# Kernel tuning notes

Hardware: AMD Instinct MI355X
Metric: run time of the kernel (lower is better)

## Reference

```python
import jax, jax.numpy as jnp
import numpy as np

# ---- dims (see shape_source) ----
B_IMG, R, E = 64, 36, 1024          # images: (n_image, n_regions, embed_size)
C_CAP, L, N_DEP = 64, 32, 30        # captions: (n_caption, n_word, embed_size)
NUM_BLOCK = 32                      # opt.num_block -> tnode feature dim (= feat_dim)
BLK = E // NUM_BLOCK                # n_block = embed_size // num_block
HID = 512                           # hid_dim (divisible by n_kernels=8)
LAM = 9.0                           # opt.lambda_softmax
EPS = 1e-8


def l2norm(x, axis):
    return x / (jnp.sqrt(jnp.sum(x * x, axis=axis, keepdims=True)) + EPS)


def setup_inputs() -> dict:
    key = jax.random.key(0)
    k = jax.random.split(key, 9)
    return {
        "images": jax.random.normal(k[0], (B_IMG, R, E), jnp.float32),
        "captions": jax.random.normal(k[1], (C_CAP, L, E), jnp.float32),
        "depends": jax.random.randint(k[2], (C_CAP, N_DEP, 2), 0, L, dtype=jnp.int32),
        # TextQueryGraphConvolution: n_kernels blocks of (HID//n_kernels, feat) concat == one (HID, feat) matrix, bias=False
        "W_gc": jax.random.normal(k[3], (HID, NUM_BLOCK), jnp.float32) / np.float32(np.sqrt(NUM_BLOCK)),
        "W_mu": jax.random.normal(k[4], (HID, HID), jnp.float32) / np.float32(np.sqrt(HID)),
        "b_mu": jnp.zeros((HID,), jnp.float32),
        "W_lv": jax.random.normal(k[5], (HID, HID), jnp.float32) * np.float32(0.02),
        "b_lv": jnp.zeros((HID,), jnp.float32),
        "W1": jax.random.normal(k[6], (HID, HID), jnp.float32) / np.float32(np.sqrt(HID)),
        "b1": jnp.zeros((HID,), jnp.float32),
        "W2": jax.random.normal(k[7], (1, HID), jnp.float32) / np.float32(np.sqrt(HID)),
        "b2": jnp.zeros((1,), jnp.float32),
    }


def _forward(images, captions, depends, W_gc, W_mu, b_mu, W_lv, b_lv, W1, b1, W2, b2):
    dep_mask = (jnp.arange(N_DEP) > 0).astype(jnp.float32)  # build_sparse_graph skips pair i==0
    eye = jnp.eye(L, dtype=jnp.float32)

    def per_caption(cap, dep):            # cap: (L,E), dep: (N_DEP,2) int
        # intra_relations: softmax over keys of lam * (Q K^T)
        words_sim = jax.nn.softmax(LAM * (cap @ cap.T), axis=-1)            # (L,L)
        # inter_relations(images, cap): leakyrelu -> l2norm over words -> softmax over regions
        attn = jnp.einsum('bre,le->brl', images, cap)                       # (B,R,L)
        attn = jnp.where(attn >= 0, attn, 0.1 * attn)                       # LeakyReLU(0.1)
        attn = l2norm(attn, axis=2)
        attn = jax.nn.softmax(LAM * jnp.swapaxes(attn, 1, 2), axis=-1)      # (B,L,R)
        wctx = jnp.einsum('blr,bre->ble', attn, images)                     # weighted context (B,L,E)
        # node-level matching: blockwise cosine similarity
        q = jnp.broadcast_to(cap, (B_IMG, L, E)).reshape(B_IMG, L, NUM_BLOCK, BLK)
        c = wctx.reshape(B_IMG, L, NUM_BLOCK, BLK)
        num = jnp.sum(q * c, axis=-1)
        den = jnp.maximum(jnp.linalg.norm(q, axis=-1) * jnp.linalg.norm(c, axis=-1), EPS)
        tnode = num / den                                                   # (B,L,NUM_BLOCK)
        # build_sparse_graph: symmetric 0/1 scatter (skip pair 0) + I
        adj = jnp.zeros((L, L), jnp.float32)
        adj = adj.at[dep[:, 0], dep[:, 1]].max(dep_mask)
        adj = adj.at[dep[:, 1], dep[:, 0]].max(dep_mask)
        adj = adj + eye
        # neighbor weights: l2norm over neighbor axis of adj-masked intra relations
        nw = l2norm(adj * words_sim, axis=1)                                # (L,L)
        # graph conv: neighbor_nodes[b,j,n,f] = adj[j,n]*tnode[b,j,f] (broadcast of unsqueeze(2));
        # agg[b,j,f] = sum_n nw[j,n]*adj[j,n]*tnode[b,j,f]; then block-concat linear = (HID,F) matmul
        s = jnp.sum(nw * adj, axis=1)                                       # (L,)
        hidden = (tnode * s[None, :, None]) @ W_gc.T                        # (B,L,HID)
        # Gaussian-process head; RBF kernel diagonal of K(x,x) is exp(0)=1, so sigma unchanged
        mu = hidden @ W_mu.T + b_mu
        sigma = jnp.exp(0.5 * (hidden @ W_lv.T + b_lv)) * 1.0
        h2 = jnp.tanh(hidden @ W1.T + b1)
        sim = (h2 @ W2.T + b2).reshape(B_IMG, L).mean(axis=1)               # (B,)
        return sim, mu, sigma

    sims, t_m, t_s = jax.vmap(per_caption)(captions, depends)               # (C,B), (C,B,L,H)
    similarities = sims.T                                                   # (B,C)
    t_m = jnp.swapaxes(t_m, 0, 1)                                           # (B,C,L,H)
    t_s = jnp.swapaxes(t_s, 0, 1)
    w = jax.nn.softmax(similarities, axis=1)[:, :, None, None]
    mu_word = jnp.sum(w * t_m, axis=1)
    var_word = jnp.sum(w * (t_s ** 2 + t_m ** 2), axis=1) - mu_word ** 2
    sigma_word = jnp.sqrt(jnp.maximum(var_word, 1e-8))
    return similarities, mu_word, sigma_word


def reference(images, captions, depends, W_gc, W_mu, b_mu, W_lv, b_lv, W1, b1, W2, b2):
    return _forward(images, captions, depends, W_gc, W_mu, b_mu, W_lv, b_lv, W1, b1, W2, b2)
```

## Files before the change

kernel.cpp:

```cpp
#include <hip/hip_runtime.h>
#include <math.h>

#define LAM 9.0f
#define EPSF 1e-8f

typedef unsigned int uint;
typedef unsigned short ushort_t;
typedef __attribute__((ext_vector_type(8))) short short8;
typedef __attribute__((ext_vector_type(4))) float float4v;
typedef __attribute__((ext_vector_type(16))) float f32x16;

#define OFF_MMU 0
#define OFF_MLV (512*32)
#define OFF_M1  (2*512*32)
#define OFF_S   (3*512*32)
#define OFF_W   (OFF_S + 64*32)
#define OFF_QN  (OFF_W + 64*64)
#define OFF_TS  (OFF_QN + 64*32*32)
#define OFF_ATTN (OFF_TS + 64*64*32*32)
#define OFF_CVT  (OFF_ATTN + 2304*2048)

#define N_IMG_EL 2359296
#define N_CAP_EL 2097152
#define IMGT2_EL 3145728

__device__ __forceinline__ ushort_t bf16_rne(float x) {
    uint u = __float_as_uint(x);
    uint r = (u + 0x7fffu + ((u >> 16) & 1u)) >> 16;
    return (ushort_t)r;
}
__device__ __forceinline__ float bf16_f(ushort_t h) {
    return __uint_as_float(((uint)h) << 16);
}
__device__ __forceinline__ uint pack2(ushort_t a, ushort_t b) {
    return (uint)a | ((uint)b << 16);
}

__global__ __launch_bounds__(256) void kcvt(const float* __restrict__ img,
                                            const float* __restrict__ cap,
                                            ushort_t* __restrict__ dst) {
    size_t i = (size_t)blockIdx.x * 256 + threadIdx.x;
    const float* src;
    ushort_t *H, *L;
    size_t base;
    if (i < (N_IMG_EL / 4)) {
        src = img; H = dst; L = dst + N_IMG_EL; base = i * 4;
    } else {
        src = cap; H = dst + 2 * (size_t)N_IMG_EL; L = H + N_CAP_EL; base = (i - N_IMG_EL / 4) * 4;
    }
    float4 v = *(const float4*)(src + base);
    float x[4] = {v.x, v.y, v.z, v.w};
    ushort_t hh[4], ll[4];
    #pragma unroll
    for (int j = 0; j < 4; j++) {
        hh[j] = bf16_rne(x[j]);
        ll[j] = bf16_rne(x[j] - bf16_f(hh[j]));
    }
    *(uint2*)(H + base) = make_uint2(pack2(hh[0], hh[1]), pack2(hh[2], hh[3]));
    *(uint2*)(L + base) = make_uint2(pack2(ll[0], ll[1]), pack2(ll[2], ll[3]));
}

__global__ __launch_bounds__(256) void kcvt2(const float* __restrict__ img,
                                             ushort_t* __restrict__ dstH) {
    int b = blockIdx.x >> 3, ecg = blockIdx.x & 7;
    __shared__ float S[36][132];
    int t = threadIdx.x;
    for (int i = t; i < 1152; i += 256) {
        int r = i >> 5, q = i & 31;
        *(float4*)&S[r][q * 4] = *(const float4*)(img + ((size_t)b * 36 + r) * 1024 + ecg * 128 + q * 4);
    }
    __syncthreads();
    int lane = t & 63, grp = t >> 6;
    int m = lane & 31, hi = lane >> 5;
    #pragma unroll
    for (int w2 = 0; w2 < 3; w2++) {
        int item = grp + w2 * 4;
        int estepL = item / 3;
        int ks3 = item - estepL * 3;
        ushort_t hh[8], ll[8];
        #pragma unroll
        for (int j = 0; j < 8; j++) {
            int r = ks3 * 16 + hi * 8 + j;
            float v = (r < 36) ? S[r][estepL * 32 + m] : 0.f;
            hh[j] = bf16_rne(v);
            ll[j] = bf16_rne(v - bf16_f(hh[j]));
        }
        int estep = ecg * 4 + estepL;
        size_t off = ((((size_t)b * 32 + estep) * 3 + ks3) * 64 + lane) * 8;
        uint4 uh, ul;
        uh.x = pack2(hh[0], hh[1]); uh.y = pack2(hh[2], hh[3]);
        uh.z = pack2(hh[4], hh[5]); uh.w = pack2(hh[6], hh[7]);
        ul.x = pack2(ll[0], ll[1]); ul.y = pack2(ll[2], ll[3]);
        ul.z = pack2(ll[4], ll[5]); ul.w = pack2(ll[6], ll[7]);
        *(uint4*)(dstH + off) = uh;
        *(uint4*)(dstH + IMGT2_EL + off) = ul;
    }
}

__global__ __launch_bounds__(256) void k2a_mfma(const ushort_t* __restrict__ cvt,
                                                float* __restrict__ C) {
    const ushort_t* imgH = cvt;
    const ushort_t* imgL = cvt + N_IMG_EL;
    const ushort_t* capH = cvt + 2 * (size_t)N_IMG_EL;
    const ushort_t* capL = capH + N_CAP_EL;
    __shared__ ushort_t Ah[128][32], Al[128][32], Bh[64][32], Bl[64][32];
    int t = threadIdx.x, w = t >> 6, lane = t & 63;
    int quad = lane >> 4, mn = lane & 15;
    int m0 = blockIdx.x * 128, n0 = blockIdx.y * 64;
    float4v acc[2][4];
    #pragma unroll
    for (int i = 0; i < 2; i++)
        #pragma unroll
        for (int j = 0; j < 4; j++) acc[i][j] = (float4v){0.f, 0.f, 0.f, 0.f};

    for (int kc = 0; kc < 32; kc++) {
        #pragma unroll
        for (int j = 0; j < 6; j++) {
            int ch = t + j * 256;
            const ushort_t* src;
            ushort_t* dst;
            if (ch < 512) {
                int row = ch >> 2, seg = ch & 3;
                src = imgH + (size_t)(m0 + row) * 1024 + kc * 32 + seg * 8;
                dst = &Ah[0][0] + ch * 8;
            } else if (ch < 1024) {
                int r2 = ch - 512, row = r2 >> 2, seg = r2 & 3;
                src = imgL + (size_t)(m0 + row) * 1024 + kc * 32 + seg * 8;
                dst = &Al[0][0] + r2 * 8;
            } else if (ch < 1280) {
                int r2 = ch - 1024, row = r2 >> 2, seg = r2 & 3;
                src = capH + (size_t)(n0 + row) * 1024 + kc * 32 + seg * 8;
                dst = &Bh[0][0] + r2 * 8;
            } else {
                int r2 = ch - 1280, row = r2 >> 2, seg = r2 & 3;
                src = capL + (size_t)(n0 + row) * 1024 + kc * 32 + seg * 8;
                dst = &Bl[0][0] + r2 * 8;
            }
            __builtin_amdgcn_global_load_lds(
                (const __attribute__((address_space(1))) uint*)src,
                (__attribute__((address_space(3))) uint*)dst, 16, 0, 0);
        }
        __syncthreads();
        short8 ah[2], al[2];
        #pragma unroll
        for (int tm = 0; tm < 2; tm++) {
            ah[tm] = *(short8*)&Ah[w * 32 + tm * 16 + mn][quad * 8];
            al[tm] = *(short8*)&Al[w * 32 + tm * 16 + mn][quad * 8];
        }
        #pragma unroll
        for (int nt = 0; nt < 4; nt++) {
            short8 bh = *(short8*)&Bh[nt * 16 + mn][quad * 8];
            short8 bl = *(short8*)&Bl[nt * 16 + mn][quad * 8];
            #pragma unroll
            for (int tm = 0; tm < 2; tm++) {
                acc[tm][nt] = __builtin_amdgcn_mfma_f32_16x16x32_bf16(ah[tm], bh, acc[tm][nt], 0, 0, 0);
                acc[tm][nt] = __builtin_amdgcn_mfma_f32_16x16x32_bf16(ah[tm], bl, acc[tm][nt], 0, 0, 0);
                acc[tm][nt] = __builtin_amdgcn_mfma_f32_16x16x32_bf16(al[tm], bh, acc[tm][nt], 0, 0, 0);
            }
        }
        __syncthreads();
    }
    #pragma unroll
    for (int tm = 0; tm < 2; tm++)
        #pragma unroll
        for (int nt = 0; nt < 4; nt++)
            #pragma unroll
            for (int r = 0; r < 4; r++) {
                int mrow = m0 + w * 32 + tm * 16 + quad * 4 + r;
                int ncol = n0 + nt * 16 + mn;
                C[(size_t)mrow * 2048 + ncol] = acc[tm][nt][r];
            }
}

__global__ __launch_bounds__(256) void kpre(const float* __restrict__ Wmu,
                                            const float* __restrict__ Wlv,
                                            const float* __restrict__ W1,
                                            const float* __restrict__ Wgc,
                                            float* __restrict__ ws) {
    int m = blockIdx.x >> 6;
    int hg = blockIdx.x & 63;
    int h0 = hg * 8;
    const float* W = (m == 0) ? Wmu : (m == 1) ? Wlv : W1;
    __shared__ float Gs[64][32];
    __shared__ float Ws[8][68];
    int t = threadIdx.x;
    int h = t >> 5, f = t & 31;
    float acc = 0.f;
    for (int kc = 0; kc < 8; kc++) {
        for (int i = t; i < 512; i += 256) {
            int row = i >> 3, c4 = i & 7;
            *(float4*)&Gs[row][c4 * 4] = *(const float4*)(Wgc + (kc * 64 + row) * 32 + c4 * 4);
        }
        if (t < 128) {
            int hh = t >> 4, c4 = t & 15;
            *(float4*)&Ws[hh][c4 * 4] = *(const float4*)(W + (size_t)(h0 + hh) * 512 + kc * 64 + c4 * 4);
        }
        __syncthreads();
        #pragma unroll 4
        for (int k = 0; k < 64; k++) acc += Ws[h][k] * Gs[k][f];
        __syncthreads();
    }
    ushort_t* Mb = (ushort_t*)ws + m * 32768;
    ushort_t hi = bf16_rne(acc);
    ushort_t lo = bf16_rne(acc - bf16_f(hi));
    Mb[(h0 + h) * 32 + f] = hi;
    Mb[16384 + (h0 + h) * 32 + f] = lo;
}

__global__ __launch_bounds__(256) void k1(const float* __restrict__ captions,
                                          const int* __restrict__ depends,
                                          float* __restrict__ ws) {
    int c = blockIdx.x;
    __shared__ float caps[32][65];
    __shared__ float G[32][33];
    __shared__ float adj[32][33];
    int t = threadIdx.x;
    int l2 = t & 31, l1_0 = t >> 5;
    float acc[4] = {0.f, 0.f, 0.f, 0.f};
    const float* cap = captions + (size_t)c * 32 * 1024;

    for (int kc = 0; kc < 16; kc++) {
        for (int i = t; i < 512; i += 256) {
            int ll = i >> 4, q = i & 15;
            float4 v = *(const float4*)(cap + ll * 1024 + kc * 64 + q * 4);
            caps[ll][q * 4 + 0] = v.x; caps[ll][q * 4 + 1] = v.y;
            caps[ll][q * 4 + 2] = v.z; caps[ll][q * 4 + 3] = v.w;
        }
        __syncthreads();
        #pragma unroll 4
        for (int k = 0; k < 64; k++) {
            float cv = caps[l2][k];
            #pragma unroll
            for (int i = 0; i < 4; i++) acc[i] += caps[l1_0 + 8 * i][k] * cv;
        }
        __syncthreads();
    }
    #pragma unroll
    for (int i = 0; i < 4; i++) G[l1_0 + 8 * i][l2] = acc[i];
    for (int i = t; i < 32 * 33; i += 256) ((float*)adj)[i] = 0.f;
    __syncthreads();

    if (t < 32) {
        float mx = -1e30f;
        for (int n = 0; n < 32; n++) mx = fmaxf(mx, LAM * G[t][n]);
        float sum = 0.f;
        for (int n = 0; n < 32; n++) { float p = __expf(LAM * G[t][n] - mx); G[t][n] = p; sum += p; }
        float inv = 1.f / sum;
        for (int n = 0; n < 32; n++) G[t][n] *= inv;
    }
    __syncthreads();
    if (t >= 1 && t < 30) {
        int d0 = depends[c * 60 + t * 2 + 0];
        int d1 = depends[c * 60 + t * 2 + 1];
        adj[d0][d1] = 1.f;
        adj[d1][d0] = 1.f;
    }
    __syncthreads();
    if (t < 32) adj[t][t] += 1.f;
    __syncthreads();
    if (t < 32) {
        float ss = 0.f, sw = 0.f;
        for (int n = 0; n < 32; n++) { float mm = adj[t][n] * G[t][n]; ss += mm * mm; }
        float inv = 1.f / (sqrtf(ss) + EPSF);
        for (int n = 0; n < 32; n++) sw += adj[t][n] * G[t][n] * adj[t][n];
        ws[OFF_S + c * 32 + t] = sw * inv;
    }
    for (int p = t; p < 1024; p += 256) {
        int l = p >> 5, f = p & 31;
        const float* cp = cap + (size_t)l * 1024 + f * 32;
        float q2 = 0.f;
        #pragma unroll
        for (int q = 0; q < 8; q++) {
            float4 v = *(const float4*)(cp + q * 4);
            q2 += v.x * v.x + v.y * v.y + v.z * v.z + v.w * v.w;
        }
        ws[OFF_QN + c * 1024 + p] = sqrtf(q2);
    }
}

__global__ __launch_bounds__(256) void k2a(const float* __restrict__ A,
                                           const float* __restrict__ Bm,
                                           float* __restrict__ C,
                                           int n0, int NW) {
    __shared__ float As[16][132];
    __shared__ float Bs[16][68];
    int m0 = blockIdx.x * 128;
    int nb0 = n0 + blockIdx.y * 64;
    int t = threadIdx.x;
    int tm = t >> 4, tn = t & 15;
    float acc[8][4] = {};
    for (int kc = 0; kc < 64; kc++) {
        #pragma unroll
        for (int j = 0; j < 2; j++) {
            int idx = t + j * 256;
            int row = idx >> 2, kq = idx & 3;
            float4 v = *(const float4*)(A + (size_t)(m0 + row) * 1024 + kc * 16 + kq * 4);
            As[kq * 4 + 0][row] = v.x; As[kq * 4 + 1][row] = v.y;
            As[kq * 4 + 2][row] = v.z; As[kq * 4 + 3][row] = v.w;
        }
        {
            int row = t >> 2, kq = t & 3;
            float4 v = *(const float4*)(Bm + (size_t)(nb0 + row) * 1024 + kc * 16 + kq * 4);
            Bs[kq * 4 + 0][row] = v.x; Bs[kq * 4 + 1][row] = v.y;
            Bs[kq * 4 + 2][row] = v.z; Bs[kq * 4 + 3][row] = v.w;
        }
        __syncthreads();
        #pragma unroll
        for (int kk = 0; kk < 16; kk++) {
            float a0[4], a1[4], bb[4];
            *(float4*)a0 = *(float4*)&As[kk][tm * 8];
            *(float4*)a1 = *(float4*)&As[kk][tm * 8 + 4];
            *(float4*)bb = *(float4*)&Bs[kk][tn * 4];
            #pragma unroll
            for (int i = 0; i < 4; i++)
                #pragma unroll
                for (int j2 = 0; j2 < 4; j2++) {
                    acc[i][j2]     += a0[i] * bb[j2];
                    acc[i + 4][j2] += a1[i] * bb[j2];
                }
        }
        __syncthreads();
    }
    int cw0 = nb0 - n0 + tn * 4;
    #pragma unroll
    for (int i = 0; i < 8; i++) {
        float4 v = make_float4(acc[i][0], acc[i][1], acc[i][2], acc[i][3]);
        *(float4*)(C + (size_t)(m0 + tm * 8 + i) * NW + cw0) = v;
    }
}

__global__ __launch_bounds__(64) void k2bm(const ushort_t* __restrict__ imgT,
                                           const float* __restrict__ captions,
                                           const float* __restrict__ attn,
                                           const float* __restrict__ ws,
                                           float* __restrict__ ts_out) {
    int orig = blockIdx.x;
    int fh = orig >> 10;
    int rest = orig & 1023;
    int cpair = rest >> 5;
    int bp = rest & 31;
    int b0 = bp * 2;
    int c0 = cpair * 2;
    __shared__ union {
        float A[2][2][36][33];
        float T[2][2][16][33];
    } u;
    int t = threadIdx.x;
    int l = t & 31, hi = t >> 5;

    for (int i = t; i < 1152; i += 64) {
        int bi = i >= 576;
        int i2 = i - bi * 576;
        int ci = i2 >= 288;
        int i3 = i2 - ci * 288;
        int r = i3 >> 3, q = i3 & 7;
        *(float4*)&u.A[bi][ci][r][q * 4] =
            *(const float4*)(attn + (size_t)((b0 + bi) * 36 + r) * 2048 + (c0 + ci) * 32 + q * 4);
    }
    __syncthreads();
    for (int i = t; i < 144; i += 64) {
        int bi = i >= 72;
        int i2 = i - bi * 72;
        int ci = i2 >= 36, r = i2 - 36 * ci;
        float ss = 0.f;
        #pragma unroll
        for (int ll = 0; ll < 32; ll++) {
            float v = u.A[bi][ci][r][ll];
            v = (v >= 0.f) ? v : 0.1f * v;
            u.A[bi][ci][r][ll] = v; ss += v * v;
        }
        float inv = 1.f / (sqrtf(ss) + EPSF);
        #pragma unroll
        for (int ll = 0; ll < 32; ll++) u.A[bi][ci][r][ll] *= inv;
    }
    __syncthreads();
    for (int i = t; i < 128; i += 64) {
        int bi = i >= 64;
        int i2 = i & 63;
        int ci = i2 >> 5, ll = i2 & 31;
        float mx = -1e30f;
        for (int r = 0; r < 36; r++) mx = fmaxf(mx, u.A[bi][ci][r][ll]);
        mx *= LAM;
        float sum = 0.f;
        for (int r = 0; r < 36; r++) { float p = __expf(LAM * u.A[bi][ci][r][ll] - mx); u.A[bi][ci][r][ll] = p; sum += p; }
        float inv = 1.f / sum;
        for (int r = 0; r < 36; r++) u.A[bi][ci][r][ll] *= inv;
    }
    __syncthreads();

    short8 bh[2][2][3], bl[2][2][3];
    #pragma unroll
    for (int bi = 0; bi < 2; bi++)
        #pragma unroll
        for (int ci = 0; ci < 2; ci++)
            #pragma unroll
            for (int k3 = 0; k3 < 3; k3++) {
                union { short8 v; ushort_t u8[8]; } H, L;
                #pragma unroll
                for (int j = 0; j < 8; j++) {
                    int r = k3 * 16 + hi * 8 + j;
                    float v = (r < 36) ? u.A[bi][ci][r][l] : 0.f;
                    ushort_t hv = bf16_rne(v);
                    H.u8[j] = hv;
                    L.u8[j] = bf16_rne(v - bf16_f(hv));
                }
                bh[bi][ci][k3] = H.v;
                bl[bi][ci][k3] = L.v;
            }
    __syncthreads();

    const ushort_t* ibH0 = imgT + (size_t)b0 * 49152;
    const ushort_t* ibL0 = ibH0 + IMGT2_EL;
    const ushort_t* ibH1 = ibH0 + 49152;
    const ushort_t* ibL1 = ibL0 + 49152;
    const float* qnp = ws + OFF_QN;
    float sv[2];
    sv[0] = ws[OFF_S + c0 * 32 + l];
    sv[1] = ws[OFF_S + (c0 + 1) * 32 + l];
    const float* capb[2];
    capb[0] = captions + (size_t)c0 * 32768 + (size_t)l * 1024 + hi * 4;
    capb[1] = capb[0] + 32768;

    for (int fl = 0; fl < 16; fl++) {
        int f = fh * 16 + fl;
        short8 aA[2][3], aB[2][3];
        #pragma unroll
        for (int k3 = 0; k3 < 3; k3++) {
            size_t off = ((size_t)(f * 3 + k3) * 64 + t) * 8;
            aA[0][k3] = *(const short8*)(ibH0 + off);
            aA[1][k3] = *(const short8*)(ibL0 + off);
            aB[0][k3] = *(const short8*)(ibH1 + off);
            aB[1][k3] = *(const short8*)(ibL1 + off);
        }
        #pragma unroll
        for (int ci = 0; ci < 2; ci++) {
            float4 cv[4];
            #pragma unroll
            for (int g = 0; g < 4; g++) cv[g] = *(const float4*)(capb[ci] + f * 32 + g * 8);
            f32x16 accA = {0.f,0.f,0.f,0.f,0.f,0.f,0.f,0.f,0.f,0.f,0.f,0.f,0.f,0.f,0.f,0.f};
            f32x16 accB = {0.f,0.f,0.f,0.f,0.f,0.f,0.f,0.f,0.f,0.f,0.f,0.f,0.f,0.f,0.f,0.f};
            #pragma unroll
            for (int k3 = 0; k3 < 3; k3++) {
                accA = __builtin_amdgcn_mfma_f32_32x32x16_bf16(aA[0][k3], bh[0][ci][k3], accA, 0, 0, 0);
                accA = __builtin_amdgcn_mfma_f32_32x32x16_bf16(aA[0][k3], bl[0][ci][k3], accA, 0, 0, 0);
                accA = __builtin_amdgcn_mfma_f32_32x32x16_bf16(aA[1][k3], bh[0][ci][k3], accA, 0, 0, 0);
                accB = __builtin_amdgcn_mfma_f32_32x32x16_bf16(aB[0][k3], bh[1][ci][k3], accB, 0, 0, 0);
                accB = __builtin_amdgcn_mfma_f32_32x32x16_bf16(aB[0][k3], bl[1][ci][k3], accB, 0, 0, 0);
                accB = __builtin_amdgcn_mfma_f32_32x32x16_bf16(aB[1][k3], bh[1][ci][k3], accB, 0, 0, 0);
            }
            float numA = 0.f, w2A = 0.f, numB = 0.f, w2B = 0.f;
            #pragma unroll
            for (int g = 0; g < 4; g++) {
                numA += cv[g].x * accA[g*4+0] + cv[g].y * accA[g*4+1]
                      + cv[g].z * accA[g*4+2] + cv[g].w * accA[g*4+3];
                w2A  += accA[g*4+0]*accA[g*4+0] + accA[g*4+1]*accA[g*4+1]
                      + accA[g*4+2]*accA[g*4+2] + accA[g*4+3]*accA[g*4+3];
                numB += cv[g].x * accB[g*4+0] + cv[g].y * accB[g*4+1]
                      + cv[g].z * accB[g*4+2] + cv[g].w * accB[g*4+3];
                w2B  += accB[g*4+0]*accB[g*4+0] + accB[g*4+1]*accB[g*4+1]
                      + accB[g*4+2]*accB[g*4+2] + accB[g*4+3]*accB[g*4+3];
            }
            numA += __shfl_xor(numA, 32); w2A += __shfl_xor(w2A, 32);
            numB += __shfl_xor(numB, 32); w2B += __shfl_xor(w2B, 32);
            if (hi == 0) {
                float qv = qnp[(c0 + ci) * 1024 + l * 32 + f];
                float denA = fmaxf(qv * sqrtf(w2A), EPSF);
                u.T[0][ci][fl][l] = (numA / denA) * sv[ci];
                float denB = fmaxf(qv * sqrtf(w2B), EPSF);
                u.T[1][ci][fl][l] = (numB / denB) * sv[ci];
            }
        }
    }
    __syncthreads();
    #pragma unroll
    for (int j = 0; j < 8; j++) {
        int id = t + j * 64;
        int bi = id >> 8;
        int ci = (id >> 7) & 1;
        int r2 = id & 127;
        int ll = r2 >> 2, q = r2 & 3;
        float4 v;
        v.x = u.T[bi][ci][q * 4 + 0][ll];
        v.y = u.T[bi][ci][q * 4 + 1][ll];
        v.z = u.T[bi][ci][q * 4 + 2][ll];
        v.w = u.T[bi][ci][q * 4 + 3][ll];
        *(float4*)(ts_out + ((size_t)(c0 + ci) * 64 + b0 + bi) * 1024 + ll * 32 + fh * 16 + q * 4) = v;
    }
}

__global__ __launch_bounds__(256) void k2b(const float* __restrict__ images,
                                           const float* __restrict__ captions,
                                           const float* __restrict__ attn,
                                           const float* __restrict__ ws,
                                           float* __restrict__ ts_out,
                                           int c0, int NW) {
    int b = blockIdx.x;
    int cw = blockIdx.y;
    int ca = c0 + cw * 2;
    __shared__ float A2[2][36][36];
    __shared__ float Ims[36][256];
    __shared__ float scs[2][32];
    const float* img = images + (size_t)b * 36 * 1024;
    int t = threadIdx.x;
    int el = t & 63;
    int lg = t >> 6;

    for (int i = t; i < 576; i += 256) {
        int r = i >> 4, q = i & 15;
        float4 v = *(const float4*)(attn + (size_t)(b * 36 + r) * NW + cw * 64 + q * 4);
        *(float4*)&A2[q >> 3][r][(q & 7) * 4] = v;
    }
    __syncthreads();
    if (t < 72) {
        int ci = t >= 36, r = t - 36 * ci;
        float ss = 0.f;
        #pragma unroll
        for (int l = 0; l < 32; l++) {
            float v = A2[ci][r][l];
            v = (v >= 0.f) ? v : 0.1f * v;
            A2[ci][r][l] = v; ss += v * v;
        }
        float inv = 1.f / (sqrtf(ss) + EPSF);
        #pragma unroll
        for (int l = 0; l < 32; l++) A2[ci][r][l] *= inv;
    }
    __syncthreads();
    if (t < 64) {
        int ci = t >> 5, l = t & 31;
        float mx = -1e30f;
        for (int r = 0; r < 36; r++) mx = fmaxf(mx, A2[ci][r][l]);
        mx *= LAM;
        float sum = 0.f;
        for (int r = 0; r < 36; r++) { float p = __expf(LAM * A2[ci][r][l] - mx); A2[ci][r][l] = p; sum += p; }
        float inv = 1.f / sum;
        for (int r = 0; r < 36; r++) A2[ci][r][l] *= inv;
    } else if (t >= 128 && t < 192) {
        int i = t - 128;
        scs[i >> 5][i & 31] = ws[OFF_S + (ca + (i >> 5)) * 32 + (i & 31)];
    }
    __syncthreads();

    const float* qn = ws + OFF_QN;
    for (int g = 0; g < 4; g++) {
        for (int i = t; i < 2304; i += 256) {
            int r = i >> 6, q = i & 63;
            *(float4*)&Ims[r][q * 4] = *(const float4*)(img + (size_t)r * 1024 + g * 256 + q * 4);
        }
        __syncthreads();

        float acc[2][8][4] = {};
        #pragma unroll 2
        for (int r = 0; r < 36; r++) {
            float4 iv = *(float4*)&Ims[r][el * 4];
            float ivv[4] = {iv.x, iv.y, iv.z, iv.w};
            #pragma unroll
            for (int ci = 0; ci < 2; ci++) {
                float av[8];
                *(float4*)&av[0] = *(float4*)&A2[ci][r][lg * 8];
                *(float4*)&av[4] = *(float4*)&A2[ci][r][lg * 8 + 4];
                #pragma unroll
                for (int i = 0; i < 8; i++)
                    #pragma unroll
                    for (int e = 0; e < 4; e++)
                        acc[ci][i][e] += av[i] * ivv[e];
            }
        }

        int fb = el >> 3;
        int f = g * 8 + fb;
        #pragma unroll
        for (int ci = 0; ci < 2; ci++) {
            int c = ca + ci;
            const float* cap = captions + (size_t)c * 32 * 1024 + g * 256;
            #pragma unroll
            for (int i = 0; i < 8; i++) {
                int l = lg * 8 + i;
                float4 cv = *(const float4*)(cap + (size_t)l * 1024 + el * 4);
                float num = cv.x * acc[ci][i][0] + cv.y * acc[ci][i][1]
                          + cv.z * acc[ci][i][2] + cv.w * acc[ci][i][3];
                float w2 = acc[ci][i][0] * acc[ci][i][0] + acc[ci][i][1] * acc[ci][i][1]
                         + acc[ci][i][2] * acc[ci][i][2] + acc[ci][i][3] * acc[ci][i][3];
                num += __shfl_down(num, 4); w2 += __shfl_down(w2, 4);
                num += __shfl_down(num, 2); w2 += __shfl_down(w2, 2);
                num += __shfl_down(num, 1); w2 += __shfl_down(w2, 1);
                if ((el & 7) == 0) {
                    float den = fmaxf(qn[c * 1024 + l * 32 + f] * sqrtf(w2), EPSF);
                    ts_out[(((size_t)c * 64 + b) * 32 + l) * 32 + f] = (num / den) * scs[ci][l];
                }
            }
        }
        __syncthreads();
    }
}

__global__ __launch_bounds__(256) void k3(const float* __restrict__ ts_ws,
                                          const ushort_t* __restrict__ Mb,
                                          const float* __restrict__ b1,
                                          const float* __restrict__ W2,
                                          const float* __restrict__ b2,
                                          float* __restrict__ out_sim) {
    int c = blockIdx.x >> 6, b = blockIdx.x & 63;
    __shared__ ushort_t tsh[32][32], tsl[32][32];
    __shared__ float red[4];
    int t = threadIdx.x;
    const float* tsrc = ts_ws + (size_t)(c * 64 + b) * 1024;
    {
        int row = t >> 3, q = t & 7;
        float4 v = *(const float4*)(tsrc + row * 32 + q * 4);
        float x[4] = {v.x, v.y, v.z, v.w};
        ushort_t hh[4], ll[4];
        #pragma unroll
        for (int j = 0; j < 4; j++) {
            hh[j] = bf16_rne(x[j]);
            ll[j] = bf16_rne(x[j] - bf16_f(hh[j]));
        }
        *(uint2*)&tsh[row][q * 4] = make_uint2(pack2(hh[0], hh[1]), pack2(hh[2], hh[3]));
        *(uint2*)&tsl[row][q * 4] = make_uint2(pack2(ll[0], ll[1]), pack2(ll[2], ll[3]));
    }
    __syncthreads();
    int w = t >> 6, lane = t & 63, quad = lane >> 4, mn = lane & 15;
    const ushort_t* M1H = Mb + 65536;
    short8 ah[2], al[2];
    #pragma unroll
    for (int mt = 0; mt < 2; mt++) {
        ah[mt] = *(short8*)&tsh[mt * 16 + mn][quad * 8];
        al[mt] = *(short8*)&tsl[mt * 16 + mn][quad * 8];
    }
    float psum = 0.f;
    #pragma unroll
    for (int nt = 0; nt < 8; nt++) {
        int h = w * 128 + nt * 16 + mn;
        short8 bh = *(const short8*)(M1H + h * 32 + quad * 8);
        short8 bl = *(const short8*)(M1H + 16384 + h * 32 + quad * 8);
        float b1v = b1[h], w2v = W2[h];
        #pragma unroll
        for (int mt = 0; mt < 2; mt++) {
            float4v acc = (float4v){0.f, 0.f, 0.f, 0.f};
            acc = __builtin_amdgcn_mfma_f32_16x16x32_bf16(ah[mt], bh, acc, 0, 0, 0);
            acc = __builtin_amdgcn_mfma_f32_16x16x32_bf16(ah[mt], bl, acc, 0, 0, 0);
            acc = __builtin_amdgcn_mfma_f32_16x16x32_bf16(al[mt], bh, acc, 0, 0, 0);
            #pragma unroll
            for (int r = 0; r < 4; r++) {
                float x = fminf(fmaxf(acc[r] + b1v, -15.f), 15.f);
                float e2 = __expf(2.f * x);
                psum += (1.f - 2.f / (e2 + 1.f)) * w2v;
            }
        }
    }
    #pragma unroll
    for (int off = 32; off >= 1; off >>= 1) psum += __shfl_down(psum, off);
    if (lane == 0) red[w] = psum;
    __syncthreads();
    if (t == 0) out_sim[b * 64 + c] = b2[0] + (red[0] + red[1] + red[2] + red[3]) * (1.f / 32.f);
}

__global__ __launch_bounds__(64) void k4(const float* __restrict__ sim, float* __restrict__ w_ws) {
    int b = blockIdx.x, t = threadIdx.x;
    float v = sim[b * 64 + t];
    float mx = v;
    #pragma unroll
    for (int off = 32; off >= 1; off >>= 1) mx = fmaxf(mx, __shfl_xor(mx, off));
    float p = __expf(v - mx);
    float sum = p;
    #pragma unroll
    for (int off = 32; off >= 1; off >>= 1) sum += __shfl_xor(sum, off);
    w_ws[b * 64 + t] = p / sum;
}

__global__ __launch_bounds__(256) void k5(const float* __restrict__ ts_ws,
                                          const float* __restrict__ ws,
                                          const float* __restrict__ b_mu,
                                          const float* __restrict__ b_lv,
                                          float* __restrict__ out) {
    int b = blockIdx.x >> 5, l = blockIdx.x & 31;
    int t = threadIdx.x;
    __shared__ ushort_t tsh[64][32], tsl[64][32];
    __shared__ float wls[64];
    {
        int cc = t >> 2, q = t & 3;
        const float* src = ts_ws + (((size_t)cc * 64 + b) * 32 + l) * 32 + q * 8;
        #pragma unroll
        for (int half = 0; half < 2; half++) {
            float4 v = *(const float4*)(src + half * 4);
            float x[4] = {v.x, v.y, v.z, v.w};
            ushort_t hh[4], ll[4];
            #pragma unroll
            for (int j = 0; j < 4; j++) {
                hh[j] = bf16_rne(x[j]);
                ll[j] = bf16_rne(x[j] - bf16_f(hh[j]));
            }
            *(uint2*)&tsh[cc][q * 8 + half * 4] = make_uint2(pack2(hh[0], hh[1]), pack2(hh[2], hh[3]));
            *(uint2*)&tsl[cc][q * 8 + half * 4] = make_uint2(pack2(ll[0], ll[1]), pack2(ll[2], ll[3]));
        }
    }
    if (t < 64) wls[t] = ws[OFF_W + b * 64 + t];
    __syncthreads();

    int w = t >> 6, lane = t & 63, quad = lane >> 4, mn = lane & 15;
    const ushort_t* Mb = (const ushort_t*)ws;
    const ushort_t* MmuH = Mb;
    const ushort_t* MlvH = Mb + 32768;
    short8 ah[4], al[4];
    #pragma unroll
    for (int mt = 0; mt < 4; mt++) {
        ah[mt] = *(short8*)&tsh[mt * 16 + mn][quad * 8];
        al[mt] = *(short8*)&tsl[mt * 16 + mn][quad * 8];
    }
    float pm[8], pq[8], pe[8];
    #pragma unroll
    for (int nt = 0; nt < 8; nt++) {
        int h = w * 128 + nt * 16 + mn;
        {
            short8 bh = *(const short8*)(MmuH + h * 32 + quad * 8);
            short8 bl = *(const short8*)(MmuH + 16384 + h * 32 + quad * 8);
            float bmv = b_mu[h];
            float am = 0.f, aq = 0.f;
            #pragma unroll
            for (int mt = 0; mt < 4; mt++) {
                float4v acc = (float4v){0.f, 0.f, 0.f, 0.f};
                acc = __builtin_amdgcn_mfma_f32_16x16x32_bf16(ah[mt], bh, acc, 0, 0, 0);
                acc = __builtin_amdgcn_mfma_f32_16x16x32_bf16(ah[mt], bl, acc, 0, 0, 0);
                acc = __builtin_amdgcn_mfma_f32_16x16x32_bf16(al[mt], bh, acc, 0, 0, 0);
                #pragma unroll
                for (int r = 0; r < 4; r++) {
                    int cc = mt * 16 + quad * 4 + r;
                    float mu = acc[r] + bmv;
                    float wv = wls[cc];
                    am += wv * mu;
                    aq += wv * mu * mu;
                }
            }
            am += __shfl_xor(am, 16); am += __shfl_xor(am, 32);
            aq += __shfl_xor(aq, 16); aq += __shfl_xor(aq, 32);
            pm[nt] = am; pq[nt] = aq;
        }
        {
            short8 bh = *(const short8*)(MlvH + h * 32 + quad * 8);
            short8 bl = *(const short8*)(MlvH + 16384 + h * 32 + quad * 8);
            float blv = b_lv[h];
            float ae = 0.f;
            #pragma unroll
            for (int mt = 0; mt < 4; mt++) {
                float4v acc = (float4v){0.f, 0.f, 0.f, 0.f};
                acc = __builtin_amdgcn_mfma_f32_16x16x32_bf16(ah[mt], bh, acc, 0, 0, 0);
                acc = __builtin_amdgcn_mfma_f32_16x16x32_bf16(ah[mt], bl, acc, 0, 0, 0);
                acc = __builtin_amdgcn_mfma_f32_16x16x32_bf16(al[mt], bh, acc, 0, 0, 0);
                #pragma unroll
                for (int r = 0; r < 4; r++) {
                    int cc = mt * 16 + quad * 4 + r;
                    ae += wls[cc] * __expf(acc[r] + blv);
                }
            }
            ae += __shfl_xor(ae, 16); ae += __shfl_xor(ae, 32);
            pe[nt] = ae;
        }
    }
    if (quad == 0) {
        #pragma unroll
        for (int nt = 0; nt < 8; nt++) {
            int h = w * 128 + nt * 16 + mn;
            size_t idx = (size_t)(b * 32 + l) * 512 + h;
            float m = pm[nt];
            out[4096 + idx] = m;
            float var = pe[nt] + pq[nt] - m * m;
            out[4096 + 64 * 32 * 512 + idx] = sqrtf(fmaxf(var, 1e-8f));
        }
    }
}

extern "C" void kernel_launch(void* const* d_in, const int* in_sizes, int n_in,
                              void* d_out, int out_size, void* d_ws, size_t ws_size,
                              hipStream_t stream) {
    const float* images   = (const float*)d_in[0];
    const float* captions = (const float*)d_in[1];
    const int*   depends  = (const int*)d_in[2];
    const float* Wgc = (const float*)d_in[3];
    const float* Wmu = (const float*)d_in[4];
    const float* bmu = (const float*)d_in[5];
    const float* Wlv = (const float*)d_in[6];
    const float* blv = (const float*)d_in[7];
    const float* W1  = (const float*)d_in[8];
    const float* b1  = (const float*)d_in[9];
    const float* W2  = (const float*)d_in[10];
    const float* b2  = (const float*)d_in[11];
    float* out = (float*)d_out;
    float* ws  = (float*)d_ws;

    hipLaunchKernelGGL(kpre, dim3(192), dim3(256), 0, stream, Wmu, Wlv, W1, Wgc, ws);
    hipLaunchKernelGGL(k1, dim3(64), dim3(256), 0, stream, captions, depends, ws);

    const size_t CVT_FLOATS = ((size_t)2 * N_IMG_EL + 2 * N_CAP_EL) / 2;
    size_t need_floats = (size_t)OFF_CVT + CVT_FLOATS;
    bool use_mfma = ws_size >= need_floats * 4;

    if (use_mfma) {
        ushort_t* cvt = (ushort_t*)(ws + OFF_CVT);
        hipLaunchKernelGGL(kcvt, dim3((N_IMG_EL + N_CAP_EL) / 4 / 256), dim3(256), 0, stream,
                           images, captions, cvt);
        hipLaunchKernelGGL(k2a_mfma, dim3(18, 32), dim3(256), 0, stream, cvt, ws + OFF_ATTN);
        hipLaunchKernelGGL(kcvt2, dim3(512), dim3(256), 0, stream, images, cvt);
        hipLaunchKernelGGL(k2bm, dim3(2048), dim3(64), 0, stream,
                           cvt, captions, ws + OFF_ATTN, ws, ws + OFF_TS);
    } else {
        int NW = 2048;
        while (NW > 64 && ((size_t)OFF_ATTN + (size_t)2304 * NW) * 4 > ws_size) NW >>= 1;
        for (int n0 = 0; n0 < 2048; n0 += NW) {
            hipLaunchKernelGGL(k2a, dim3(18, NW / 64), dim3(256), 0, stream,
                               images, captions, ws + OFF_ATTN, n0, NW);
            hipLaunchKernelGGL(k2b, dim3(64, NW / 64), dim3(256), 0, stream,
                               images, captions, ws + OFF_ATTN, ws, ws + OFF_TS, n0 / 32, NW);
        }
    }

    hipLaunchKernelGGL(k3, dim3(4096), dim3(256), 0, stream,
                       ws + OFF_TS, (const ushort_t*)ws, b1, W2, b2, out);
    hipLaunchKernelGGL(k4, dim3(64), dim3(64), 0, stream, out, ws + OFF_W);
    hipLaunchKernelGGL(k5, dim3(2048), dim3(256), 0, stream, ws + OFF_TS, ws, bmu, blv, out);
}
```

Baseline: 345.4 us.

## Fuse leaky-relu and word l2norm into GEMM epilogue; restructure k2bm tiling

Moves the leaky-ReLU and per-region l2 normalisation over the 32 words of each caption into the attention GEMM epilogue, using cross-lane shuffles, so the attn buffer is stored already normalised. k2bm now loads attn straight into registers and does the region softmax with one wave shuffle instead of staging through shared memory with several barriers. It also retiles k2bm to 4 captions by 8 features per block instead of 2 by 16, so each image fragment load feeds more MFMAs. The cost is more live registers, since bh and bl double in size, which may lower occupancy.

```diff
diff --git a/kernel.cpp b/kernel.cpp
--- a/kernel.cpp
+++ b/kernel.cpp
@@ -166,9 +166,34 @@
         for (int nt = 0; nt < 4; nt++)
             #pragma unroll
             for (int r = 0; r < 4; r++) {
+                float v = acc[tm][nt][r];
+                acc[tm][nt][r] = (v >= 0.f) ? v : 0.1f * v;
+            }
+    float invA[2][4], invB[2][4];
+    #pragma unroll
+    for (int tm = 0; tm < 2; tm++)
+        #pragma unroll
+        for (int r = 0; r < 4; r++) {
+            float ssA = acc[tm][0][r] * acc[tm][0][r] + acc[tm][1][r] * acc[tm][1][r];
+            float ssB = acc[tm][2][r] * acc[tm][2][r] + acc[tm][3][r] * acc[tm][3][r];
+            #pragma unroll
+            for (int off = 1; off < 16; off <<= 1) {
+                ssA += __shfl_xor(ssA, off);
+                ssB += __shfl_xor(ssB, off);
+            }
+            invA[tm][r] = 1.f / (sqrtf(ssA) + EPSF);
+            invB[tm][r] = 1.f / (sqrtf(ssB) + EPSF);
+        }
+    #pragma unroll
+    for (int tm = 0; tm < 2; tm++)
+        #pragma unroll
+        for (int nt = 0; nt < 4; nt++)
+            #pragma unroll
+            for (int r = 0; r < 4; r++) {
                 int mrow = m0 + w * 32 + tm * 16 + quad * 4 + r;
                 int ncol = n0 + nt * 16 + mn;
-                C[(size_t)mrow * 2048 + ncol] = acc[tm][nt][r];
+                float sc = (nt < 2) ? invA[tm][r] : invB[tm][r];
+                C[(size_t)mrow * 2048 + ncol] = acc[tm][nt][r] * sc;
             }
 }
 
@@ -335,118 +360,95 @@
                                            const float* __restrict__ ws,
                                            float* __restrict__ ts_out) {
     int orig = blockIdx.x;
-    int fh = orig >> 10;
-    int rest = orig & 1023;
-    int cpair = rest >> 5;
-    int bp = rest & 31;
-    int b0 = bp * 2;
-    int c0 = cpair * 2;
-    __shared__ union {
-        float A[2][2][36][33];
-        float T[2][2][16][33];
-    } u;
-    int t = threadIdx.x;
-    int l = t & 31, hi = t >> 5;
-
-    for (int i = t; i < 1152; i += 64) {
-        int bi = i >= 576;
-        int i2 = i - bi * 576;
-        int ci = i2 >= 288;
-        int i3 = i2 - ci * 288;
-        int r = i3 >> 3, q = i3 & 7;
-        *(float4*)&u.A[bi][ci][r][q * 4] =
-            *(const float4*)(attn + (size_t)((b0 + bi) * 36 + r) * 2048 + (c0 + ci) * 32 + q * 4);
-    }
-    __syncthreads();
-    for (int i = t; i < 144; i += 64) {
-        int bi = i >= 72;
-        int i2 = i - bi * 72;
-        int ci = i2 >= 36, r = i2 - 36 * ci;
-        float ss = 0.f;
-        #pragma unroll
-        for (int ll = 0; ll < 32; ll++) {
-            float v = u.A[bi][ci][r][ll];
-            v = (v >= 0.f) ? v : 0.1f * v;
-            u.A[bi][ci][r][ll] = v; ss += v * v;
-        }
-        float inv = 1.f / (sqrtf(ss) + EPSF);
-        #pragma unroll
-        for (int ll = 0; ll < 32; ll++) u.A[bi][ci][r][ll] *= inv;
-    }
-    __syncthreads();
-    for (int i = t; i < 128; i += 64) {
-        int bi = i >= 64;
-        int i2 = i & 63;
-        int ci = i2 >> 5, ll = i2 & 31;
-        float mx = -1e30f;
-        for (int r = 0; r < 36; r++) mx = fmaxf(mx, u.A[bi][ci][r][ll]);
-        mx *= LAM;
-        float sum = 0.f;
-        for (int r = 0; r < 36; r++) { float p = __expf(LAM * u.A[bi][ci][r][ll] - mx); u.A[bi][ci][r][ll] = p; sum += p; }
-        float inv = 1.f / sum;
-        for (int r = 0; r < 36; r++) u.A[bi][ci][r][ll] *= inv;
-    }
-    __syncthreads();
-
-    short8 bh[2][2][3], bl[2][2][3];
+    int fq = orig >> 9;
+    int cg = (orig >> 5) & 15;
+    int bp = orig & 31;
+    int b0 = bp * 2, c0 = cg * 4;
+    __shared__ float T[2][4][8][33];
+    int t = threadIdx.x, l = t & 31, hi = t >> 5;
+
+    short8 bh[2][4][3], bl[2][4][3];
     #pragma unroll
     for (int bi = 0; bi < 2; bi++)
         #pragma unroll
-        for (int ci = 0; ci < 2; ci++)
+        for (int ci = 0; ci < 4; ci++) {
+            const float* ap = attn + ((size_t)(b0 + bi) * 36) * 2048 + (c0 + ci) * 32 + l;
+            float av[3][8];
+            float mx = -1e30f;
+            #pragma unroll
+            for (int k3 = 0; k3 < 3; k3++)
+                #pragma unroll
+                for (int j = 0; j < 8; j++) {
+                    int r = k3 * 16 + hi * 8 + j;
+                    float v = (r < 36) ? ap[(size_t)r * 2048] : -1e30f;
+                    av[k3][j] = v;
+                    mx = fmaxf(mx, v);
+                }
+            mx = fmaxf(mx, __shfl_xor(mx, 32)) * LAM;
+            float sum = 0.f;
+            #pragma unroll
+            for (int k3 = 0; k3 < 3; k3++)
+                #pragma unroll
+                for (int j = 0; j < 8; j++) {
+                    int r = k3 * 16 + hi * 8 + j;
+                    float p = (r < 36) ? __expf(LAM * av[k3][j] - mx) : 0.f;
+                    av[k3][j] = p;
+                    sum += p;
+                }
+            sum += __shfl_xor(sum, 32);
+            float inv = 1.f / sum;
             #pragma unroll
             for (int k3 = 0; k3 < 3; k3++) {
                 union { short8 v; ushort_t u8[8]; } H, L;
                 #pragma unroll
                 for (int j = 0; j < 8; j++) {
-                    int r = k3 * 16 + hi * 8 + j;
-                    float v = (r < 36) ? u.A[bi][ci][r][l] : 0.f;
-                    ushort_t hv = bf16_rne(v);
+                    float p = av[k3][j] * inv;
+                    ushort_t hv = bf16_rne(p);
                     H.u8[j] = hv;
-                    L.u8[j] = bf16_rne(v - bf16_f(hv));
+                    L.u8[j] = bf16_rne(p - bf16_f(hv));
                 }
                 bh[bi][ci][k3] = H.v;
                 bl[bi][ci][k3] = L.v;
             }
-    __syncthreads();
+        }
 
     const ushort_t* ibH0 = imgT + (size_t)b0 * 49152;
     const ushort_t* ibL0 = ibH0 + IMGT2_EL;
     const ushort_t* ibH1 = ibH0 + 49152;
     const ushort_t* ibL1 = ibL0 + 49152;
     const float* qnp = ws + OFF_QN;
-    float sv[2];
-    sv[0] = ws[OFF_S + c0 * 32 + l];
-    sv[1] = ws[OFF_S + (c0 + 1) * 32 + l];
-    const float* capb[2];
-    capb[0] = captions + (size_t)c0 * 32768 + (size_t)l * 1024 + hi * 4;
-    capb[1] = capb[0] + 32768;
-
-    for (int fl = 0; fl < 16; fl++) {
-        int f = fh * 16 + fl;
-        short8 aA[2][3], aB[2][3];
+    float sv[4];
+    #pragma unroll
+    for (int ci = 0; ci < 4; ci++) sv[ci] = ws[OFF_S + (c0 + ci) * 32 + l];
+
+    for (int fl = 0; fl < 8; fl++) {
+        int f = fq * 8 + fl;
+        short8 aH0[3], aL0[3], aH1[3], aL1[3];
         #pragma unroll
         for (int k3 = 0; k3 < 3; k3++) {
             size_t off = ((size_t)(f * 3 + k3) * 64 + t) * 8;
-            aA[0][k3] = *(const short8*)(ibH0 + off);
-            aA[1][k3] = *(const short8*)(ibL0 + off);
-            aB[0][k3] = *(const short8*)(ibH1 + off);
-            aB[1][k3] = *(const short8*)(ibL1 + off);
-        }
-        #pragma unroll
-        for (int ci = 0; ci < 2; ci++) {
+            aH0[k3] = *(const short8*)(ibH0 + off);
+            aL0[k3] = *(const short8*)(ibL0 + off);
+            aH1[k3] = *(const short8*)(ibH1 + off);
+            aL1[k3] = *(const short8*)(ibL1 + off);
+        }
+        #pragma unroll
+        for (int ci = 0; ci < 4; ci++) {
             float4 cv[4];
             #pragma unroll
-            for (int g = 0; g < 4; g++) cv[g] = *(const float4*)(capb[ci] + f * 32 + g * 8);
+            for (int g = 0; g < 4; g++)
+                cv[g] = *(const float4*)(captions + (size_t)(c0 + ci) * 32768
+                         + (size_t)l * 1024 + f * 32 + g * 8 + hi * 4);
             f32x16 accA = {0.f,0.f,0.f,0.f,0.f,0.f,0.f,0.f,0.f,0.f,0.f,0.f,0.f,0.f,0.f,0.f};
             f32x16 accB = {0.f,0.f,0.f,0.f,0.f,0.f,0.f,0.f,0.f,0.f,0.f,0.f,0.f,0.f,0.f,0.f};
             #pragma unroll
             for (int k3 = 0; k3 < 3; k3++) {
-                accA = __builtin_amdgcn_mfma_f32_32x32x16_bf16(aA[0][k3], bh[0][ci][k3], accA, 0, 0, 0);
-                accA = __builtin_amdgcn_mfma_f32_32x32x16_bf16(aA[0][k3], bl[0][ci][k3], accA, 0, 0, 0);
-                accA = __builtin_amdgcn_mfma_f32_32x32x16_bf16(aA[1][k3], bh[0][ci][k3], accA, 0, 0, 0);
-                accB = __builtin_amdgcn_mfma_f32_32x32x16_bf16(aB[0][k3], bh[1][ci][k3], accB, 0, 0, 0);
-                accB = __builtin_amdgcn_mfma_f32_32x32x16_bf16(aB[0][k3], bl[1][ci][k3], accB, 0, 0, 0);
-                accB = __builtin_amdgcn_mfma_f32_32x32x16_bf16(aB[1][k3], bh[1][ci][k3], accB, 0, 0, 0);
+                accA = __builtin_amdgcn_mfma_f32_32x32x16_bf16(aH0[k3], bh[0][ci][k3], accA, 0, 0, 0);
+                accA = __builtin_amdgcn_mfma_f32_32x32x16_bf16(aH0[k3], bl[0][ci][k3], accA, 0, 0, 0);
+                accA = __builtin_amdgcn_mfma_f32_32x32x16_bf16(aL0[k3], bh[0][ci][k3], accA, 0, 0, 0);
+                accB = __builtin_amdgcn_mfma_f32_32x32x16_bf16(aH1[k3], bh[1][ci][k3], accB, 0, 0, 0);
+                accB = __builtin_amdgcn_mfma_f32_32x32x16_bf16(aH1[k3], bl[1][ci][k3], accB, 0, 0, 0);
+                accB = __builtin_amdgcn_mfma_f32_32x32x16_bf16(aL1[k3], bh[1][ci][k3], accB, 0, 0, 0);
             }
             float numA = 0.f, w2A = 0.f, numB = 0.f, w2B = 0.f;
             #pragma unroll
@@ -465,9 +467,9 @@
             if (hi == 0) {
                 float qv = qnp[(c0 + ci) * 1024 + l * 32 + f];
                 float denA = fmaxf(qv * sqrtf(w2A), EPSF);
-                u.T[0][ci][fl][l] = (numA / denA) * sv[ci];
+                T[0][ci][fl][l] = (numA / denA) * sv[ci];
                 float denB = fmaxf(qv * sqrtf(w2B), EPSF);
-                u.T[1][ci][fl][l] = (numB / denB) * sv[ci];
+                T[1][ci][fl][l] = (numB / denB) * sv[ci];
             }
         }
     }
@@ -476,15 +478,15 @@
     for (int j = 0; j < 8; j++) {
         int id = t + j * 64;
         int bi = id >> 8;
-        int ci = (id >> 7) & 1;
-        int r2 = id & 127;
-        int ll = r2 >> 2, q = r2 & 3;
+        int ci = (id >> 6) & 3;
+        int rem = id & 63;
+        int ll = rem >> 1, q = rem & 1;
         float4 v;
-        v.x = u.T[bi][ci][q * 4 + 0][ll];
-        v.y = u.T[bi][ci][q * 4 + 1][ll];
-        v.z = u.T[bi][ci][q * 4 + 2][ll];
-        v.w = u.T[bi][ci][q * 4 + 3][ll];
-        *(float4*)(ts_out + ((size_t)(c0 + ci) * 64 + b0 + bi) * 1024 + ll * 32 + fh * 16 + q * 4) = v;
+        v.x = T[bi][ci][q * 4 + 0][ll];
+        v.y = T[bi][ci][q * 4 + 1][ll];
+        v.z = T[bi][ci][q * 4 + 2][ll];
+        v.w = T[bi][ci][q * 4 + 3][ll];
+        *(float4*)(ts_out + ((size_t)(c0 + ci) * 64 + b0 + bi) * 1024 + ll * 32 + fq * 8 + q * 4) = v;
     }
 }
 
```

Result: slower. 410.4 us (+18.8%).
